# Kernel tuning notes

Measured on AMD Instinct MI355X. Metric: run time of the kernel, lower is better.

## Reference

```python
import jax, jax.numpy as jnp
import numpy as np
from jax.scipy.special import logsumexp

B, L, M, D = 8192, 1024, 128, 2  # batch, hilbert.size, bond dim, local_size
MACHINE_POW = 2


def setup_inputs() -> dict:
    key = jax.random.key(0)
    k1, k2 = jax.random.split(key)
    # configurations in the zero-magnetization sector: each row is a permutation
    # of L//2 zeros and L//2 ones (constrained HomogeneousHilbert)
    base = jnp.tile(jnp.arange(D, dtype=jnp.int32), L // D)  # (L,)
    inputs = jax.vmap(lambda k: jax.random.permutation(k, base))(jax.random.split(k1, B))
    # variational parameters epsilon: (local_size, M, size); centered at 1 so the
    # length-L multiplicative cache chain stays in fp32 range
    epsilon = 1.0 + 0.02 * jax.random.normal(k2, (D, M, L), dtype=jnp.float32)
    return {"inputs": inputs, "epsilon": epsilon}


def _conditionals(inputs, epsilon):
    # inputs: (B, L) int in [0, D); epsilon: (D, M, L)
    Bn, Ln = inputs.shape
    Dn, Mn, _ = epsilon.shape
    half = Ln // 2

    def scan_fun(carry, index):
        cache, n_spins = carry                       # (B, D, M), (B, D)
        prev = inputs[:, (index - 1) % Ln]           # (B,) previous-site state
        params_i = epsilon[:, :, index]              # (D, M)
        # irregular gather: cache[b, prev[b], :]
        gathered = jnp.take_along_axis(cache, prev[:, None, None], axis=1)[:, 0, :]  # (B, M)
        prods = params_i[None, :, :] * gathered[:, None, :]  # (B, D, M)
        log_psi = jnp.sum(prods, axis=-1)            # (B, D) sum over bond dim
        n_spins = jnp.where(index > 0,
                            n_spins + jax.nn.one_hot(prev, Dn, dtype=jnp.int32),
                            n_spins)
        # zero-magnetization renormalization: -inf once a local state is exhausted
        renorm = jnp.log(jnp.heaviside((half - n_spins).astype(log_psi.dtype), 0.0))
        return (prods, n_spins), log_psi + renorm

    cache0 = jnp.ones((Bn, Dn, Mn), epsilon.dtype)
    n0 = jnp.zeros((Bn, Dn), jnp.int32)
    _, log_psi = jax.lax.scan(scan_fun, (cache0, n0), jnp.arange(Ln))
    return jnp.transpose(log_psi, (1, 0, 2))  # (B, L, D)


def reference(inputs, epsilon):
    lp = _conditionals(inputs, epsilon)  # (B, L, D)
    # normalize conditionals over local states (machine_pow = 2)
    lp = lp - (1.0 / MACHINE_POW) * logsumexp(MACHINE_POW * lp, axis=-1, keepdims=True)
    # pick the log-conditional of the actual configuration at each site
    sel = jnp.take_along_axis(lp, inputs[:, :, None], axis=2)[:, :, 0]  # (B, L)
    # n_symm = 1 (default apply_symmetries): symmetrized logsumexp is identity
    return jnp.sum(sel, axis=1)  # (B,) log_psi
```

## Files before the change

kernel.cpp:

```cpp
#include <hip/hip_runtime.h>

typedef unsigned long long u64;
typedef unsigned int uint32;
typedef short short8 __attribute__((ext_vector_type(8)));
typedef float f32x4 __attribute__((ext_vector_type(4)));
typedef float f32x2 __attribute__((ext_vector_type(2)));

#define B_N 8192
#define L_N 1024
#define M_N 128
#define C_N 16
#define CH_N 64
#define HALF_N 512
#define SL 20
#define ROWF (8 * SL)

#define OFF_W    0
#define OFF_R    0x80000
#define OFF_BITS 0x100000
#define OFF_LR   0x208000
#define OFF_RQ   0x248000

__device__ __forceinline__ unsigned short f32_bf16(float f) {
    union { float f; unsigned u; } x; x.f = f;
    unsigned u = x.u + 0x7FFFu + ((x.u >> 16) & 1u);
    return (unsigned short)(u >> 16);
}
__device__ __forceinline__ float bf16lo(uint32 w) {
    union { unsigned u; float f; } x; x.u = w << 16; return x.f;
}
__device__ __forceinline__ float bf16hi(uint32 w) {
    union { unsigned u; float f; } x; x.u = w & 0xFFFF0000u; return x.f;
}

__global__ __launch_bounds__(256) void k_pack(const int* __restrict__ inp, u64* __restrict__ bits) {
    int g = blockIdx.x * 256 + threadIdx.x;
    int v = inp[g];
    u64 m = __ballot(v != 0);
    if ((threadIdx.x & 63) == 0) bits[g >> 6] = m;
}

__global__ __launch_bounds__(64) void k_eps(const float* __restrict__ eps,
        float* __restrict__ w, float* __restrict__ r, unsigned short* __restrict__ lrT) {
    int m = blockIdx.x, lane = threadIdx.x;
    const float* e0 = eps + (size_t)m * L_N + lane * 16;
    const float* e1 = eps + (size_t)(M_N + m) * L_N + lane * 16;
    float a[16], b[16];
    #pragma unroll
    for (int j = 0; j < 16; j += 4) {
        *(float4*)&a[j] = *(const float4*)&e0[j];
        *(float4*)&b[j] = *(const float4*)&e1[j];
    }
    float local = 1.f;
    #pragma unroll
    for (int j = 0; j < 16; ++j) local *= a[j];
    float sc = local;
    #pragma unroll
    for (int d = 1; d < 64; d <<= 1) {
        float up = __shfl_up(sc, d);
        if (lane >= d) sc *= up;
    }
    float prev = __shfl_up(sc, 1);
    float E = (lane == 0) ? 1.f : prev;
    int i0 = lane * 16;
    #pragma unroll
    for (int j = 0; j < 16; ++j) {
        float rat = b[j] / a[j];
        w[(size_t)(i0 + j) * M_N + m] = E * (a[j] - b[j]);
        r[(size_t)(i0 + j) * M_N + m] = rat;
        lrT[(size_t)m * L_N + i0 + j] = f32_bf16(__log2f(rat));
        E *= a[j];
    }
}

__global__ __launch_bounds__(256) void k_slog2(const u64* __restrict__ bits,
        const unsigned short* __restrict__ lrT, unsigned short* __restrict__ Rq) {
    int btile = blockIdx.x >> 1;
    int half = blockIdx.x & 1;
    int wid = threadIdx.x >> 6, lane = threadIdx.x & 63;
    int col = lane & 15, quad = lane >> 4;
    int m = (half * 4 + wid) * 16 + col;
    int b_row = btile * 16 + col;
    const u64* brow = bits + (size_t)b_row * 16;
    const unsigned short* lrow = lrT + (size_t)m * L_N;

    f32x4 cum = (f32x4){0.f, 0.f, 0.f, 0.f};

    for (int c = 0; c < C_N; ++c) {
        #pragma unroll
        for (int reg = 0; reg < 4; ++reg) {
            int b = btile * 16 + quad * 4 + reg;
            Rq[((size_t)c * B_N + b) * M_N + m] = f32_bf16(exp2f(cum[reg]));
        }
        u64 wv = brow[c];
        short8 a0, a1;
        #pragma unroll
        for (int j = 0; j < 8; ++j) {
            a0[j] = (short)((((wv >> (quad * 8 + j)) & 1) != 0) ? 0x3F80 : 0);
            a1[j] = (short)((((wv >> (32 + quad * 8 + j)) & 1) != 0) ? 0x3F80 : 0);
        }
        const unsigned short* bp = lrow + c * 64 + quad * 8;
        union { uint4 u; short8 s; } bf0, bf1;
        bf0.u = *(const uint4*)bp;
        bf1.u = *(const uint4*)(bp + 32);
        cum = __builtin_amdgcn_mfma_f32_16x16x32_bf16(a0, bf0.s, cum, 0, 0, 0);
        cum = __builtin_amdgcn_mfma_f32_16x16x32_bf16(a1, bf1.s, cum, 0, 0, 0);
    }
}

__global__ __launch_bounds__(256, 4) void k_main(const u64* __restrict__ bits,
        const float* __restrict__ w, const float* __restrict__ r,
        const unsigned short* __restrict__ Rq, float* __restrict__ out) {
    __shared__ float wbuf[32 * ROWF];
    __shared__ float rbuf[32 * ROWF];
    int c = blockIdx.x & (C_N - 1);
    int bblk = blockIdx.x >> 4;
    int lane = threadIdx.x & 63, wid = threadIdx.x >> 6;
    int s = lane & 7, g = lane >> 3;
    int b0 = bblk * 128 + wid * 32 + g * 4;
    int b_own = b0 + (s & 3);

    f32x2 R2[4][8];
    #pragma unroll
    for (int nb = 0; nb < 4; ++nb) {
        const uint4* src = (const uint4*)(Rq + ((size_t)c * B_N + (b0 + nb)) * M_N + s * 16);
        #pragma unroll
        for (int u_ = 0; u_ < 2; ++u_) {
            uint4 pv = src[u_];
            R2[nb][u_ * 4 + 0] = (f32x2){bf16lo(pv.x), bf16hi(pv.x)};
            R2[nb][u_ * 4 + 1] = (f32x2){bf16lo(pv.y), bf16hi(pv.y)};
            R2[nb][u_ * 4 + 2] = (f32x2){bf16lo(pv.z), bf16hi(pv.z)};
            R2[nb][u_ * 4 + 3] = (f32x2){bf16lo(pv.w), bf16hi(pv.w)};
        }
    }
    int n1 = 0;
    for (int k = 0; k < c; ++k) n1 += __popcll(bits[(size_t)b_own * 16 + k]);
    int n0 = c * CH_N - n1;

    float sum = 0.f;
    for (int h = 0; h < 2; ++h) {
        __syncthreads();
        const float4* srcw = (const float4*)(w + ((size_t)c * CH_N + h * 32) * M_N);
        const float4* srcr = (const float4*)(r + ((size_t)c * CH_N + h * 32) * M_N);
        for (int t = threadIdx.x; t < 32 * 32; t += 256) {
            int i = t >> 5, mqd = t & 31;
            int dst = i * ROWF + (mqd >> 2) * SL + (mqd & 3) * 4;
            *(float4*)&wbuf[dst] = srcw[t];
            *(float4*)&rbuf[dst] = srcr[t];
        }
        __syncthreads();

        uint32 wh[4];
        #pragma unroll
        for (int nb = 0; nb < 4; ++nb)
            wh[nb] = (uint32)(bits[(size_t)(b0 + nb) * 16 + c] >> (h * 32));
        uint32 owa = (s & 1) ? wh[1] : wh[0];
        uint32 owb = (s & 1) ? wh[3] : wh[2];
        uint32 ow = (s & 2) ? owb : owa;

        for (int tt = 0; tt < 32; ++tt) {
            int base = tt * ROWF + s * SL;
            const f32x2* wp = (const f32x2*)&wbuf[base];
            f32x2 w2[8];
            #pragma unroll
            for (int j = 0; j < 8; ++j) w2[j] = wp[j];

            float d[4];
            #pragma unroll
            for (int nb = 0; nb < 4; ++nb) {
                f32x2 acc = R2[nb][0] * w2[0];
                #pragma unroll
                for (int j = 1; j < 8; ++j) acc += R2[nb][j] * w2[j];
                d[nb] = acc[0] + acc[1];
            }
            #pragma unroll
            for (int nb = 0; nb < 4; ++nb) {
                d[nb] += __shfl_xor(d[nb], 1);
                d[nb] += __shfl_xor(d[nb], 2);
            }
            int sb3 = s & 3;
            float sel = d[0];
            if (sb3 == 1) sel = d[1];
            if (sb3 == 2) sel = d[2];
            if (sb3 == 3) sel = d[3];
            sel += __shfl_xor(sel, 4);
            float Dv = sel;

            int sbit = (ow >> tt) & 1;
            bool valid = (n0 < HALF_N) && (n1 < HALF_N);
            float ad = fabsf(Dv);
            float contr = -fmaxf(sbit ? Dv : -Dv, 0.f)
                          - 0.5f * __logf(1.f + __expf(-2.f * ad));
            sum += valid ? contr : 0.f;
            n1 += sbit; n0 += 1 - sbit;

            const f32x2* rp = (const f32x2*)&rbuf[base];
            f32x2 r2[8];
            #pragma unroll
            for (int j = 0; j < 8; ++j) r2[j] = rp[j];
            #pragma unroll
            for (int nb = 0; nb < 4; ++nb) {
                if ((wh[nb] >> tt) & 1) {
                    #pragma unroll
                    for (int j = 0; j < 8; ++j) R2[nb][j] *= r2[j];
                }
            }
        }
    }
    if (s < 4) atomicAdd(&out[b_own], sum);
}

extern "C" void kernel_launch(void* const* d_in, const int* in_sizes, int n_in,
                              void* d_out, int out_size, void* d_ws, size_t ws_size,
                              hipStream_t stream) {
    const int*   inputs  = (const int*)d_in[0];
    const float* epsilon = (const float*)d_in[1];
    float* out = (float*)d_out;

    char* ws = (char*)d_ws;
    float* w_tab  = (float*)(ws + OFF_W);
    float* r_tab  = (float*)(ws + OFF_R);
    u64*   bits   = (u64*)  (ws + OFF_BITS);
    unsigned short* lrT = (unsigned short*)(ws + OFF_LR);
    unsigned short* Rq  = (unsigned short*)(ws + OFF_RQ);

    k_pack<<<(B_N * L_N) / 256, 256, 0, stream>>>(inputs, bits);
    k_eps<<<M_N, 64, 0, stream>>>(epsilon, w_tab, r_tab, lrT);
    hipMemsetAsync(d_out, 0, B_N * sizeof(float), stream);
    k_slog2<<<(B_N / 16) * 2, 256, 0, stream>>>(bits, lrT, Rq);
    k_main<<<(B_N / 128) * C_N, 256, 0, stream>>>(bits, w_tab, r_tab, Rq, out);
}
```

Baseline: 196.8 us.

## Split bond dimension across 16 lanes per batch group, halving per-thread state

Each group of four batch rows is now handled by 16 lanes instead of 8, so every lane holds 8 bond entries per row instead of 16 and the grid doubles. The reduction becomes a transpose-style butterfly exchange, so fewer shuffles run per step. Shared-memory reads switch to 128-bit loads, and the softplus is rewritten in a form with fewer instructions. The intent is fewer registers and more occupancy and parallelism, at the cost of more blocks re-staging the same w/r tables. The new softplus form may also overflow for large positive arguments.

```diff
diff --git a/kernel.cpp b/kernel.cpp
--- a/kernel.cpp
+++ b/kernel.cpp
@@ -116,22 +116,18 @@
     int c = blockIdx.x & (C_N - 1);
     int bblk = blockIdx.x >> 4;
     int lane = threadIdx.x & 63, wid = threadIdx.x >> 6;
-    int s = lane & 7, g = lane >> 3;
-    int b0 = bblk * 128 + wid * 32 + g * 4;
+    int s = lane & 15, g = lane >> 4;
+    int b0 = bblk * 64 + wid * 16 + g * 4;
     int b_own = b0 + (s & 3);
 
-    f32x2 R2[4][8];
+    f32x2 R2[4][4];
     #pragma unroll
     for (int nb = 0; nb < 4; ++nb) {
-        const uint4* src = (const uint4*)(Rq + ((size_t)c * B_N + (b0 + nb)) * M_N + s * 16);
-        #pragma unroll
-        for (int u_ = 0; u_ < 2; ++u_) {
-            uint4 pv = src[u_];
-            R2[nb][u_ * 4 + 0] = (f32x2){bf16lo(pv.x), bf16hi(pv.x)};
-            R2[nb][u_ * 4 + 1] = (f32x2){bf16lo(pv.y), bf16hi(pv.y)};
-            R2[nb][u_ * 4 + 2] = (f32x2){bf16lo(pv.z), bf16hi(pv.z)};
-            R2[nb][u_ * 4 + 3] = (f32x2){bf16lo(pv.w), bf16hi(pv.w)};
-        }
+        uint4 pv = *(const uint4*)(Rq + ((size_t)c * B_N + (b0 + nb)) * M_N + s * 8);
+        R2[nb][0] = (f32x2){bf16lo(pv.x), bf16hi(pv.x)};
+        R2[nb][1] = (f32x2){bf16lo(pv.y), bf16hi(pv.y)};
+        R2[nb][2] = (f32x2){bf16lo(pv.z), bf16hi(pv.z)};
+        R2[nb][3] = (f32x2){bf16lo(pv.w), bf16hi(pv.w)};
     }
     int n1 = 0;
     for (int k = 0; k < c; ++k) n1 += __popcll(bits[(size_t)b_own * 16 + k]);
@@ -158,51 +154,55 @@
         uint32 owb = (s & 1) ? wh[3] : wh[2];
         uint32 ow = (s & 2) ? owb : owa;
 
+        int lbase0 = (s >> 1) * SL + (s & 1) * 8;
+
         for (int tt = 0; tt < 32; ++tt) {
-            int base = tt * ROWF + s * SL;
-            const f32x2* wp = (const f32x2*)&wbuf[base];
-            f32x2 w2[8];
-            #pragma unroll
-            for (int j = 0; j < 8; ++j) w2[j] = wp[j];
+            int base = tt * ROWF + lbase0;
+            f32x4 wa = *(const f32x4*)&wbuf[base];
+            f32x4 wb2 = *(const f32x4*)&wbuf[base + 4];
+            f32x2 w20 = (f32x2){wa[0], wa[1]},  w21 = (f32x2){wa[2], wa[3]};
+            f32x2 w22 = (f32x2){wb2[0], wb2[1]}, w23 = (f32x2){wb2[2], wb2[3]};
 
             float d[4];
             #pragma unroll
             for (int nb = 0; nb < 4; ++nb) {
-                f32x2 acc = R2[nb][0] * w2[0];
-                #pragma unroll
-                for (int j = 1; j < 8; ++j) acc += R2[nb][j] * w2[j];
+                f32x2 acc = R2[nb][0] * w20;
+                acc += R2[nb][1] * w21;
+                acc += R2[nb][2] * w22;
+                acc += R2[nb][3] * w23;
                 d[nb] = acc[0] + acc[1];
             }
-            #pragma unroll
-            for (int nb = 0; nb < 4; ++nb) {
-                d[nb] += __shfl_xor(d[nb], 1);
-                d[nb] += __shfl_xor(d[nb], 2);
-            }
-            int sb3 = s & 3;
-            float sel = d[0];
-            if (sb3 == 1) sel = d[1];
-            if (sb3 == 2) sel = d[2];
-            if (sb3 == 3) sel = d[3];
-            sel += __shfl_xor(sel, 4);
-            float Dv = sel;
+            float xa = (s & 1) ? d[1] : d[0];
+            float ya = (s & 1) ? d[0] : d[1];
+            xa += __shfl_xor(ya, 1);
+            float xb = (s & 1) ? d[3] : d[2];
+            float yb = (s & 1) ? d[2] : d[3];
+            xb += __shfl_xor(yb, 1);
+            float u = (s & 2) ? xb : xa;
+            float v = (s & 2) ? xa : xb;
+            u += __shfl_xor(v, 2);
+            u += __shfl_xor(u, 4);
+            u += __shfl_xor(u, 8);
+            float Dv = u;
 
             int sbit = (ow >> tt) & 1;
             bool valid = (n0 < HALF_N) && (n1 < HALF_N);
-            float ad = fabsf(Dv);
-            float contr = -fmaxf(sbit ? Dv : -Dv, 0.f)
-                          - 0.5f * __logf(1.f + __expf(-2.f * ad));
+            float y = sbit ? Dv : -Dv;
+            float contr = -0.5f * __logf(1.f + __expf(2.f * y));
             sum += valid ? contr : 0.f;
             n1 += sbit; n0 += 1 - sbit;
 
-            const f32x2* rp = (const f32x2*)&rbuf[base];
-            f32x2 r2[8];
-            #pragma unroll
-            for (int j = 0; j < 8; ++j) r2[j] = rp[j];
+            f32x4 ra = *(const f32x4*)&rbuf[base];
+            f32x4 rb2 = *(const f32x4*)&rbuf[base + 4];
+            f32x2 r20 = (f32x2){ra[0], ra[1]},  r21 = (f32x2){ra[2], ra[3]};
+            f32x2 r22 = (f32x2){rb2[0], rb2[1]}, r23 = (f32x2){rb2[2], rb2[3]};
             #pragma unroll
             for (int nb = 0; nb < 4; ++nb) {
                 if ((wh[nb] >> tt) & 1) {
-                    #pragma unroll
-                    for (int j = 0; j < 8; ++j) R2[nb][j] *= r2[j];
+                    R2[nb][0] *= r20;
+                    R2[nb][1] *= r21;
+                    R2[nb][2] *= r22;
+                    R2[nb][3] *= r23;
                 }
             }
         }
@@ -228,5 +228,5 @@
     k_eps<<<M_N, 64, 0, stream>>>(epsilon, w_tab, r_tab, lrT);
     hipMemsetAsync(d_out, 0, B_N * sizeof(float), stream);
     k_slog2<<<(B_N / 16) * 2, 256, 0, stream>>>(bits, lrT, Rq);
-    k_main<<<(B_N / 128) * C_N, 256, 0, stream>>>(bits, w_tab, r_tab, Rq, out);
-}
+    k_main<<<(B_N / 64) * C_N, 256, 0, stream>>>(bits, w_tab, r_tab, Rq, out);
+}
```

Measured after the change: 223.8 us. +13.7%, slower.
